# Kernel tuning notes

Measured on AMD Instinct MI355X. Metric: run time of the kernel, lower is better.

Reference implementation:

```python
import jax, jax.numpy as jnp
import numpy as np


def _grid_sample_bilinear_zeros(img, grid):
    """PyTorch grid_sample(mode='bilinear', padding_mode='zeros', align_corners=True).
    img: (N, C, H, W); grid: (N, Ho, Wo, 2) with last dim = (x_norm, y_norm) in [-1, 1].
    """
    N, C, H, W = img.shape
    gx = (grid[..., 0] + 1.0) * 0.5 * (W - 1)  # (N, Ho, Wo) pixel coords
    gy = (grid[..., 1] + 1.0) * 0.5 * (H - 1)
    x0 = jnp.floor(gx)
    y0 = jnp.floor(gy)
    x1 = x0 + 1.0
    y1 = y0 + 1.0
    wx1 = gx - x0
    wx0 = 1.0 - wx1
    wy1 = gy - y0
    wy0 = 1.0 - wy1

    def corner(xi, yi, wgt):
        valid = ((xi >= 0) & (xi <= W - 1) & (yi >= 0) & (yi <= H - 1)).astype(img.dtype)
        xc = jnp.clip(xi, 0, W - 1).astype(jnp.int32)
        yc = jnp.clip(yi, 0, H - 1).astype(jnp.int32)
        # per-sample fancy gather: (C,H,W)[ :, (Ho,Wo), (Ho,Wo)] -> (C,Ho,Wo)
        v = jax.vmap(lambda im, yy, xx: im[:, yy, xx])(img, yc, xc)  # (N,C,Ho,Wo)
        return v * (valid * wgt)[:, None]

    return (corner(x0, y0, wx0 * wy0) + corner(x1, y0, wx1 * wy0)
            + corner(x0, y1, wx0 * wy1) + corner(x1, y1, wx1 * wy1))


def _backwarp(x, flow):
    """x, flow: (N, C/2, H, W); flow in pixels (hor, ver). align_corners=True grid."""
    N, _, H, W = flow.shape
    hor = jnp.linspace(-1.0, 1.0, W, dtype=flow.dtype)
    ver = jnp.linspace(-1.0, 1.0, H, dtype=flow.dtype)
    base = jnp.stack([jnp.broadcast_to(hor[None, :], (H, W)),
                      jnp.broadcast_to(ver[:, None], (H, W))], axis=0)[None]  # (1,2,H,W)
    # pixel flow -> normalized flow (H != W branch of original)
    norm = jnp.array([2.0 / (W - 1.0), 2.0 / (H - 1.0)], dtype=flow.dtype).reshape(1, 2, 1, 1)
    g = (base + flow * norm).transpose(0, 2, 3, 1)  # (N,H,W,2)
    return _grid_sample_bilinear_zeros(x, g)


def setup_inputs() -> dict:
    key = jax.random.key(0)
    k1, k2 = jax.random.split(key)
    B, C, T, H, W = 2, 3, 5, 720, 1280
    x = jax.random.normal(k1, (B, C, T, H, W), dtype=jnp.float32)
    f = jax.random.normal(k2, (B, 3, T, H, W), dtype=jnp.float32)
    return {"x": x, "f": f}


def reference(x, f):
    # scale = 1, num_seq = T (interpolate branch skipped since scale == 1)
    B, C, T, H, W = x.shape
    xf = x.transpose(0, 2, 1, 3, 4).reshape(B * T, C, H, W)      # (b t) c h w
    ff = f.transpose(0, 2, 1, 3, 4).reshape(B * T, 3, H, W)
    weight = jax.nn.sigmoid(ff[:, 2:3])                           # (BT,1,H,W)
    flow = ff[:, :2]                                              # (BT,2,H,W)
    xw = _backwarp(xf, flow)                                      # warped image
    ow = _backwarp(jnp.ones_like(xf), flow) * weight              # warped ones mask
    xw = xw * weight
    def back(a):  # (b t) c h w -> b c t h w
        return a.reshape(B, T, a.shape[1], H, W).transpose(0, 2, 1, 3, 4)
    return (back(ow), back(xw))
```

## Files before the change

kernel.cpp:

```cpp
#include <hip/hip_runtime.h>

constexpr int B  = 2, C = 3, T = 5, H = 720, W = 1280;
constexpr int HW = H * W;
constexpr int W4 = W / 4;
constexpr int P4 = B * T * H * W4;
constexpr int CH_STRIDE = T * HW;
constexpr int OUT_HALF  = B * C * T * HW;
constexpr int NBLK   = P4 / 256;
constexpr int ROWBLK = (H * W4) / 256;
constexpr int NXCD   = 8;
constexpr int CHUNK  = NBLK / NXCD;

typedef float2 __attribute__((aligned(4))) f2u;

__global__ __launch_bounds__(256, 4)
void bwarp_kernel(const float* __restrict__ x, const float* __restrict__ f,
                  float* __restrict__ out)
{
    int bid = blockIdx.x;
    int swz = (bid & (NXCD - 1)) * CHUNK + (bid >> 3);

    int btu = __builtin_amdgcn_readfirstlane(swz / ROWBLK);
    int i2  = (swz - btu * ROWBLK) * 256 + (int)threadIdx.x;
    int b   = btu / T, t = btu - b * T;
    int plane = (b * 3 * T + t) * HW;

    int w4i = i2 % W4;
    int h   = i2 / W4;
    int base0 = plane + h * W + 4 * w4i;

    float4 fx4 = *(const float4*)(f + base0);
    float4 fy4 = *(const float4*)(f + base0 + CH_STRIDE);
    float4 fw4 = *(const float4*)(f + base0 + 2 * CH_STRIDE);
    const float* fxp = (const float*)&fx4;
    const float* fyp = (const float*)&fy4;
    const float* fwp = (const float*)&fw4;

    int   a0[4], a1[4];
    float wA[4], wB[4], wC[4], wD[4], sig[4], o0[4];

    #pragma unroll
    for (int j = 0; j < 4; ++j) {
        float gx = (float)(4 * w4i + j) + fxp[j];
        float gy = (float)h + fyp[j];

        float x0f = floorf(gx), y0f = floorf(gy);
        float wx1 = gx - x0f, wx0 = 1.0f - wx1;
        float wy1 = gy - y0f, wy0 = 1.0f - wy1;
        int x0 = (int)x0f, y0 = (int)y0f;
        int x1 = x0 + 1,   y1 = y0 + 1;

        float vx0 = (x0 >= 0 && x0 < W) ? 1.0f : 0.0f;
        float vx1 = (x1 >= 0 && x1 < W) ? 1.0f : 0.0f;
        float vy0 = (y0 >= 0 && y0 < H) ? 1.0f : 0.0f;
        float vy1 = (y1 >= 0 && y1 < H) ? 1.0f : 0.0f;

        float w00 = wx0 * wy0 * vx0 * vy0;
        float w10 = wx1 * wy0 * vx1 * vy0;
        float w01 = wx0 * wy1 * vx0 * vy1;
        float w11 = wx1 * wy1 * vx1 * vy1;

        float s = 1.0f / (1.0f + __expf(-fwp[j]));
        sig[j] = s;
        o0[j]  = (w00 + w10 + w01 + w11) * s;

        bool edge = (x0 < 0) | (x0 >= W - 1);
        wA[j] = edge ? w10 : w00;
        wB[j] = edge ? w00 : w10;
        wC[j] = edge ? w11 : w01;
        wD[j] = edge ? w01 : w11;

        int xl  = min(max(x0, 0), W - 2);
        int y0c = min(max(y0, 0), H - 1);
        int y1c = min(max(y1, 0), H - 1);
        a0[j] = y0c * W + xl;
        a1[j] = y1c * W + xl;
    }

    f2u p0[3][4], p1[3][4];
    #pragma unroll
    for (int c = 0; c < 3; ++c) {
        const float* xp = x + plane + c * CH_STRIDE;
        #pragma unroll
        for (int j = 0; j < 4; ++j) {
            p0[c][j] = *(const f2u*)(xp + a0[j]);
            p1[c][j] = *(const f2u*)(xp + a1[j]);
        }
    }

    float4 ow4 = make_float4(o0[0], o0[1], o0[2], o0[3]);
    #pragma unroll
    for (int c = 0; c < 3; ++c) {
        float r[4];
        #pragma unroll
        for (int j = 0; j < 4; ++j) {
            float v = wA[j] * p0[c][j].x;
            v = fmaf(wB[j], p0[c][j].y, v);
            v = fmaf(wC[j], p1[c][j].x, v);
            v = fmaf(wD[j], p1[c][j].y, v);
            r[j] = v * sig[j];
        }
        *(float4*)(out + base0 + c * CH_STRIDE) = ow4;
        *(float4*)(out + OUT_HALF + base0 + c * CH_STRIDE)
            = make_float4(r[0], r[1], r[2], r[3]);
    }
}

extern "C" void kernel_launch(void* const* d_in, const int* in_sizes, int n_in,
                              void* d_out, int out_size, void* d_ws, size_t ws_size,
                              hipStream_t stream) {
    const float* x = (const float*)d_in[0];
    const float* f = (const float*)d_in[1];
    float* out = (float*)d_out;
    bwarp_kernel<<<NBLK, 256, 0, stream>>>(x, f, out);
}
```

Before: 407.8 us.

## Map blocks to 2D 32x16 pixel tiles with two pixels per thread

Each block now covers a 2D tile 32 pixels wide and 16 rows tall, with each thread handling 2 pixels, instead of a linear 1024-pixel row strip with 4 pixels per thread. With random flow, the gathers from neighbouring rows are meant to land in overlapping cache lines within a block, improving L1/L2 reuse. The trade-off is narrower float2 loads and stores instead of float4, twice as many blocks, and shorter contiguous row segments per wavefront.

```diff
diff --git a/kernel.cpp b/kernel.cpp
--- a/kernel.cpp
+++ b/kernel.cpp
@@ -2,14 +2,17 @@
 
 constexpr int B  = 2, C = 3, T = 5, H = 720, W = 1280;
 constexpr int HW = H * W;
-constexpr int W4 = W / 4;
-constexpr int P4 = B * T * H * W4;
 constexpr int CH_STRIDE = T * HW;
 constexpr int OUT_HALF  = B * C * T * HW;
-constexpr int NBLK   = P4 / 256;
-constexpr int ROWBLK = (H * W4) / 256;
-constexpr int NXCD   = 8;
-constexpr int CHUNK  = NBLK / NXCD;
+
+constexpr int TILE_W = 16;
+constexpr int TILE_H = 16;
+constexpr int TPW = (W / 2) / TILE_W;
+constexpr int TPC = H / TILE_H;
+constexpr int TPP = TPW * TPC;
+constexpr int NBLK  = B * T * TPP;
+constexpr int NXCD  = 8;
+constexpr int CHUNK = NBLK / NXCD;
 
 typedef float2 __attribute__((aligned(4))) f2u;
 
@@ -20,29 +23,34 @@
     int bid = blockIdx.x;
     int swz = (bid & (NXCD - 1)) * CHUNK + (bid >> 3);
 
-    int btu = __builtin_amdgcn_readfirstlane(swz / ROWBLK);
-    int i2  = (swz - btu * ROWBLK) * 256 + (int)threadIdx.x;
+    int btu = __builtin_amdgcn_readfirstlane(swz / TPP);
+    int rem = swz - btu * TPP;
+    int ty  = __builtin_amdgcn_readfirstlane(rem / TPW);
+    int tx  = rem - ty * TPW;
     int b   = btu / T, t = btu - b * T;
     int plane = (b * 3 * T + t) * HW;
 
-    int w4i = i2 % W4;
-    int h   = i2 / W4;
-    int base0 = plane + h * W + 4 * w4i;
+    int lx = (int)threadIdx.x & (TILE_W - 1);
+    int ly = (int)threadIdx.x >> 4;
+    int xpx = (tx * TILE_W + lx) * 2;
+    int h   = ty * TILE_H + ly;
+    int base0 = plane + h * W + xpx;
 
-    float4 fx4 = *(const float4*)(f + base0);
-    float4 fy4 = *(const float4*)(f + base0 + CH_STRIDE);
-    float4 fw4 = *(const float4*)(f + base0 + 2 * CH_STRIDE);
-    const float* fxp = (const float*)&fx4;
-    const float* fyp = (const float*)&fy4;
-    const float* fwp = (const float*)&fw4;
+    float2 fx2 = *(const float2*)(f + base0);
+    float2 fy2 = *(const float2*)(f + base0 + CH_STRIDE);
+    float2 fw2 = *(const float2*)(f + base0 + 2 * CH_STRIDE);
 
-    int   a0[4], a1[4];
-    float wA[4], wB[4], wC[4], wD[4], sig[4], o0[4];
+    int   a0[2], a1[2];
+    float wA[2], wB[2], wC[2], wD[2], sig[2], o0[2];
 
     #pragma unroll
-    for (int j = 0; j < 4; ++j) {
-        float gx = (float)(4 * w4i + j) + fxp[j];
-        float gy = (float)h + fyp[j];
+    for (int j = 0; j < 2; ++j) {
+        float fx = j ? fx2.y : fx2.x;
+        float fy = j ? fy2.y : fy2.x;
+        float fw = j ? fw2.y : fw2.x;
+
+        float gx = (float)(xpx + j) + fx;
+        float gy = (float)h + fy;
 
         float x0f = floorf(gx), y0f = floorf(gy);
         float wx1 = gx - x0f, wx0 = 1.0f - wx1;
@@ -60,7 +68,7 @@
         float w01 = wx0 * wy1 * vx0 * vy1;
         float w11 = wx1 * wy1 * vx1 * vy1;
 
-        float s = 1.0f / (1.0f + __expf(-fwp[j]));
+        float s = 1.0f / (1.0f + __expf(-fw));
         sig[j] = s;
         o0[j]  = (w00 + w10 + w01 + w11) * s;
 
@@ -77,32 +85,32 @@
         a1[j] = y1c * W + xl;
     }
 
-    f2u p0[3][4], p1[3][4];
+    f2u p0[3][2], p1[3][2];
     #pragma unroll
     for (int c = 0; c < 3; ++c) {
         const float* xp = x + plane + c * CH_STRIDE;
         #pragma unroll
-        for (int j = 0; j < 4; ++j) {
+        for (int j = 0; j < 2; ++j) {
             p0[c][j] = *(const f2u*)(xp + a0[j]);
             p1[c][j] = *(const f2u*)(xp + a1[j]);
         }
     }
 
-    float4 ow4 = make_float4(o0[0], o0[1], o0[2], o0[3]);
+    float2 ow2 = make_float2(o0[0], o0[1]);
     #pragma unroll
     for (int c = 0; c < 3; ++c) {
-        float r[4];
+        float r[2];
         #pragma unroll
-        for (int j = 0; j < 4; ++j) {
+        for (int j = 0; j < 2; ++j) {
             float v = wA[j] * p0[c][j].x;
             v = fmaf(wB[j], p0[c][j].y, v);
             v = fmaf(wC[j], p1[c][j].x, v);
             v = fmaf(wD[j], p1[c][j].y, v);
             r[j] = v * sig[j];
         }
-        *(float4*)(out + base0 + c * CH_STRIDE) = ow4;
-        *(float4*)(out + OUT_HALF + base0 + c * CH_STRIDE)
-            = make_float4(r[0], r[1], r[2], r[3]);
+        *(float2*)(out + base0 + c * CH_STRIDE) = ow2;
+        *(float2*)(out + OUT_HALF + base0 + c * CH_STRIDE)
+            = make_float2(r[0], r[1]);
     }
 }
 
```

New measurement: 380.8 us. -6.6%, faster.
